# Performance work log

Measured on AMD Instinct MI355X. Metric: run time of the kernel, lower is better.

Reference implementation:

```python
import jax, jax.numpy as jnp
import numpy as np

HID, SD, EXP, DTR = 1024, 16, 2048, 64
B_, T_ = 4, 2048


def setup_inputs() -> dict:
    key = jax.random.key(0)
    ks = jax.random.split(key, 9)
    def rn(k, shape, s=0.02):
        return jax.random.normal(k, shape, jnp.float32) * s
    return {
        "x": jax.random.normal(ks[0], (B_, T_, HID), jnp.float32),
        "ln_g": jnp.ones((HID,), jnp.float32),
        "ln_b": jnp.zeros((HID,), jnp.float32),
        "W_in": rn(ks[1], (HID, 2 * EXP)),
        "b_in": jnp.zeros((2 * EXP,), jnp.float32),
        "W_del": rn(ks[2], (EXP, DTR)),
        "b_del": jnp.zeros((DTR,), jnp.float32),
        "W_dt": rn(ks[3], (DTR, EXP)),
        "b_dt": jnp.zeros((EXP,), jnp.float32),
        "W_B": rn(ks[4], (EXP, SD)),
        "b_B": jnp.zeros((SD,), jnp.float32),
        "W_C": rn(ks[5], (EXP, SD)),
        "b_C": jnp.zeros((SD,), jnp.float32),
        "A_log": -jnp.exp(0.1 * jax.random.normal(ks[6], (EXP, SD), jnp.float32)),
        "Dp": jnp.zeros((EXP,), jnp.float32),
        "W_out": rn(ks[7], (EXP, HID)),
        "b_out": jnp.zeros((HID,), jnp.float32),
    }


def _layernorm(x, g, b, eps=1e-5):
    m = jnp.mean(x, axis=-1, keepdims=True)
    v = jnp.var(x, axis=-1, keepdims=True)
    return (x - m) * jax.lax.rsqrt(v + eps) * g + b


def _selective_scan(u, delta, A, Bm, Cm):
    # u, delta: (B,T,E); Bm, Cm: (B,T,Sd); A: (E,Sd)
    def step(h, inp):
        u_t, d_t, B_t, C_t = inp  # (B,E),(B,E),(B,Sd),(B,Sd)
        A_disc = jnp.exp(d_t[..., None] * A[None])          # (B,E,Sd)
        h = A_disc * h + d_t[..., None] * B_t[:, None, :] * u_t[..., None]
        y_t = jnp.einsum("bs,bds->bd", C_t, h)
        return h, y_t
    h0 = jnp.zeros((u.shape[0], u.shape[2], A.shape[1]), u.dtype)
    xs = (u.transpose(1, 0, 2), delta.transpose(1, 0, 2),
          Bm.transpose(1, 0, 2), Cm.transpose(1, 0, 2))
    _, ys = jax.lax.scan(step, h0, xs)  # ys: (T,B,E)
    return ys.transpose(1, 0, 2)


def reference(x, ln_g, ln_b, W_in, b_in, W_del, b_del, W_dt, b_dt,
              W_B, b_B, W_C, b_C, A_log, Dp, W_out, b_out):
    res = x
    xn = _layernorm(x, ln_g, ln_b)
    xp = xn @ W_in + b_in                 # (B,T,2E)
    u, gate = jnp.split(xp, 2, axis=-1)   # each (B,T,E)
    u = jax.nn.silu(u)
    delta = jax.nn.softplus((u @ W_del + b_del) @ W_dt + b_dt)  # (B,T,E)
    Bm = u @ W_B + b_B                    # (B,T,Sd)
    Cm = u @ W_C + b_C                    # (B,T,Sd)
    A = -jnp.exp(A_log)                   # (E,Sd)
    y = _selective_scan(u, delta, A, Bm, Cm)
    y = y + u * Dp
    y = y * jax.nn.silu(gate)
    return y @ W_out + b_out + res
```

## Files before the change

kernel.cpp:

```cpp
#include <hip/hip_runtime.h>

#define HIDN 1024
#define EXPN 2048
#define SDIM 16
#define DTRN 64
#define BBN  4
#define TTN  2048
#define MMN  (BBN*TTN)
#define NCHUNK 32
#define CLEN (TTN/NCHUNK)
#define KSPL 8
#define KCH  (EXPN/KSPL)

typedef unsigned short u16;
typedef __bf16 bf16x8 __attribute__((ext_vector_type(8)));
typedef float f32x4 __attribute__((ext_vector_type(4)));

static __device__ __forceinline__ float b2f(u16 u) {
    union { unsigned int i; float f; } cv; cv.i = ((unsigned int)u) << 16; return cv.f;
}
static __device__ __forceinline__ u16 f2b(float f) {
    union { float f; unsigned int i; } cv; cv.f = f;
    unsigned int x = cv.i;
    return (u16)((x + 0x7fffu + ((x >> 16) & 1u)) >> 16);
}
static __device__ __forceinline__ float fexp2(float x) {
    return __builtin_amdgcn_exp2f(x);
}

static __device__ __forceinline__
void tr_tile(const float* __restrict__ W, u16* __restrict__ Wt,
             int K, int N, int bk, int bn, float (*t)[65]) {
    const int r0 = threadIdx.x >> 4, c0 = (threadIdx.x & 15) << 2;
    #pragma unroll
    for (int i = 0; i < 4; ++i) {
        float4 v = *(const float4*)(W + (size_t)(bk + r0 + i * 16) * N + bn + c0);
        t[r0 + i * 16][c0 + 0] = v.x; t[r0 + i * 16][c0 + 1] = v.y;
        t[r0 + i * 16][c0 + 2] = v.z; t[r0 + i * 16][c0 + 3] = v.w;
    }
    __syncthreads();
    #pragma unroll
    for (int i = 0; i < 4; ++i) {
        const int n = r0 + i * 16;
        ushort4 o;
        o.x = f2b(t[c0 + 0][n]); o.y = f2b(t[c0 + 1][n]);
        o.z = f2b(t[c0 + 2][n]); o.w = f2b(t[c0 + 3][n]);
        *(ushort4*)(Wt + (size_t)(bn + n) * K + bk + c0) = o;
    }
}

__global__ __launch_bounds__(256)
void k_prep(const float* __restrict__ W_in, const float* __restrict__ W_out,
            const float* __restrict__ W_dt, const float* __restrict__ W_del,
            const float* __restrict__ W_B, const float* __restrict__ W_C,
            const float* __restrict__ A_log,
            u16* __restrict__ Wt_in, u16* __restrict__ Wt_out,
            u16* __restrict__ Wdt_t, u16* __restrict__ Wcat,
            float* __restrict__ A2) {
    __shared__ float t[64][65];
    int blk = blockIdx.x;
    if (blk < 1024) {
        tr_tile(W_in, Wt_in, HIDN, 2 * EXPN, (blk >> 6) << 6, (blk & 63) << 6, t);
        return;
    }
    blk -= 1024;
    if (blk < 512) {
        tr_tile(W_out, Wt_out, EXPN, HIDN, (blk >> 4) << 6, (blk & 15) << 6, t);
        return;
    }
    blk -= 512;
    if (blk < 32) {
        tr_tile(W_dt, Wdt_t, DTRN, EXPN, 0, blk << 6, t);
        return;
    }
    blk -= 32;
    if (blk < 768) {
        const int i = blk * 256 + threadIdx.x;
        const int n = i >> 11, k = i & 2047;
        float v;
        if (n < 64)      v = W_del[(size_t)k * DTRN + n];
        else if (n < 80) v = W_B[(size_t)k * SDIM + (n - 64)];
        else             v = W_C[(size_t)k * SDIM + (n - 80)];
        Wcat[i] = f2b(v);
        return;
    }
    blk -= 768;
    {
        const int i = blk * 256 + threadIdx.x;
        A2[i] = -__expf(A_log[i]) * 1.44269504088896340736f;
    }
}

__global__ __launch_bounds__(256) void k_ln(const float* __restrict__ x,
                                            const float* __restrict__ g,
                                            const float* __restrict__ bta,
                                            u16* __restrict__ xn) {
    const int row = blockIdx.x, tid = threadIdx.x;
    const float4 xv = ((const float4*)(x + (size_t)row * HIDN))[tid];
    float s  = xv.x + xv.y + xv.z + xv.w;
    float ss = fmaf(xv.x, xv.x, fmaf(xv.y, xv.y, fmaf(xv.z, xv.z, xv.w * xv.w)));
    #pragma unroll
    for (int o = 32; o > 0; o >>= 1) { s += __shfl_down(s, o); ss += __shfl_down(ss, o); }
    __shared__ float as[4], bs[4];
    const int wid = tid >> 6, lane = tid & 63;
    if (lane == 0) { as[wid] = s; bs[wid] = ss; }
    __syncthreads();
    const float S  = as[0] + as[1] + as[2] + as[3];
    const float SS = bs[0] + bs[1] + bs[2] + bs[3];
    const float mean = S * (1.f / HIDN);
    const float var  = SS * (1.f / HIDN) - mean * mean;
    const float r = rsqrtf(var + 1e-5f);
    const float4 gv = ((const float4*)g)[tid];
    const float4 bv = ((const float4*)bta)[tid];
    ushort4 o;
    o.x = f2b((xv.x - mean) * r * gv.x + bv.x);
    o.y = f2b((xv.y - mean) * r * gv.y + bv.y);
    o.z = f2b((xv.z - mean) * r * gv.z + bv.z);
    o.w = f2b((xv.w - mean) * r * gv.w + bv.w);
    ((ushort4*)(xn + (size_t)row * HIDN))[tid] = o;
}

#define MEPI_SPLIT_SILU 0
#define MEPI_OUT        1
#define MEPI_SP         2

static __device__ __forceinline__
void stage256(const u16* __restrict__ A, const u16* __restrict__ Bt,
              u16 (*seg)[8192], int brow, int bcol, int K, int k0,
              const int* srow, const int* scol, int tid) {
    #pragma unroll
    for (int j = 0; j < 2; ++j) {
        #pragma unroll
        for (int h = 0; h < 2; ++h) {
            const u16* sa = A + (size_t)(brow + h * 128 + srow[j]) * K + k0 + scol[j];
            __builtin_amdgcn_global_load_lds(
                (const __attribute__((address_space(1))) void*)sa,
                (__attribute__((address_space(3))) void*)&seg[h][(j * 512 + tid) * 8], 16, 0, 0);
            const u16* sb = Bt + (size_t)(bcol + h * 128 + srow[j]) * K + k0 + scol[j];
            __builtin_amdgcn_global_load_lds(
                (const __attribute__((address_space(1))) void*)sb,
                (__attribute__((address_space(3))) void*)&seg[2 + h][(j * 512 + tid) * 8], 16, 0, 0);
        }
    }
}

template<int EPI>
__global__ __launch_bounds__(512, 2)
void mgemm256(const u16* __restrict__ A, const u16* __restrict__ Bt,
              const float* __restrict__ bias, void* __restrict__ O0,
              void* __restrict__ O1, const float* __restrict__ res,
              int N, int K) {
    __shared__ u16 lds[2][4][8192];
    const int tid  = threadIdx.x;
    const int lane = tid & 63, wid = tid >> 6;
    const int wm = wid >> 2, wn = wid & 3;
    const int r  = lane & 15, kh = lane >> 4;
    const int brow = blockIdx.y * 256, bcol = blockIdx.x * 256;

    int srow[2], scol[2];
    #pragma unroll
    for (int j = 0; j < 2; ++j) {
        const int q = j * 512 + tid;
        const int sub = q >> 6, qi = q & 63;
        const int qis = qi ^ (((qi >> 5) & 1) << 1);
        srow[j] = (sub >> 1) * 16 + (qi >> 2);
        scol[j] = ((sub & 1) << 5) + (qis & 3) * 8;
    }
    const int swz_kh = kh ^ (((r >> 3) & 1) << 1);
    const int rbase  = r * 32 + swz_kh * 8;
    const int bq     = wn & 1;

    f32x4 acc[8][4];
    #pragma unroll
    for (int i = 0; i < 8; ++i)
        #pragma unroll
        for (int n = 0; n < 4; ++n) acc[i][n] = (f32x4){0.f, 0.f, 0.f, 0.f};

    const int NT = K >> 6;
    stage256(A, Bt, lds[0], brow, bcol, K, 0, srow, scol, tid);
    stage256(A, Bt, lds[1], brow, bcol, K, 64, srow, scol, tid);
    asm volatile("s_waitcnt vmcnt(8)" ::: "memory");
    __builtin_amdgcn_s_barrier();
    asm volatile("" ::: "memory");

    bf16x8 a[4][2], b[2][2][2];
    for (int kt = 0; kt < NT; ++kt) {
        const u16* segA = lds[kt & 1][wm];
        const u16* segB = lds[kt & 1][2 + (wn >> 1)];
        #pragma unroll
        for (int mf = 0; mf < 4; ++mf)
            #pragma unroll
            for (int kk = 0; kk < 2; ++kk)
                a[mf][kk] = *(const bf16x8*)&segA[(mf * 2 + kk) * 512 + rbase];
        #pragma unroll
        for (int nf = 0; nf < 2; ++nf)
            #pragma unroll
            for (int kk = 0; kk < 2; ++kk)
                b[0][nf][kk] = *(const bf16x8*)&segB[((bq * 4 + nf) * 2 + kk) * 512 + rbase];
        __builtin_amdgcn_s_barrier(); asm volatile("" ::: "memory");
        __builtin_amdgcn_s_setprio(1);
        #pragma unroll
        for (int mf = 0; mf < 4; ++mf)
            #pragma unroll
            for (int nf = 0; nf < 2; ++nf)
                #pragma unroll
                for (int kk = 0; kk < 2; ++kk)
                    acc[mf][nf] = __builtin_amdgcn_mfma_f32_16x16x32_bf16(a[mf][kk], b[0][nf][kk], acc[mf][nf], 0, 0, 0);
        __builtin_amdgcn_s_setprio(0);
        __builtin_amdgcn_s_barrier(); asm volatile("" ::: "memory");
        #pragma unroll
        for (int nf = 0; nf < 2; ++nf)
            #pragma unroll
            for (int kk = 0; kk < 2; ++kk)
                b[1][nf][kk] = *(const bf16x8*)&segB[((bq * 4 + 2 + nf) * 2 + kk) * 512 + rbase];
        __builtin_amdgcn_s_barrier(); asm volatile("" ::: "memory");
        __builtin_amdgcn_s_setprio(1);
        #pragma unroll
        for (int mf = 0; mf < 4; ++mf)
            #pragma unroll
            for (int nf = 0; nf < 2; ++nf)
                #pragma unroll
                for (int kk = 0; kk < 2; ++kk)
                    acc[mf][2 + nf] = __builtin_amdgcn_mfma_f32_16x16x32_bf16(a[mf][kk], b[1][nf][kk], acc[mf][2 + nf], 0, 0, 0);
        __builtin_amdgcn_s_setprio(0);
        __builtin_amdgcn_s_barrier(); asm volatile("" ::: "memory");
        #pragma unroll
        for (int mf = 0; mf < 4; ++mf)
            #pragma unroll
            for (int kk = 0; kk < 2; ++kk)
                a[mf][kk] = *(const bf16x8*)&segA[((4 + mf) * 2 + kk) * 512 + rbase];
        __builtin_amdgcn_s_barrier(); asm volatile("" ::: "memory");
        __builtin_amdgcn_s_setprio(1);
        #pragma unroll
        for (int mf = 0; mf < 4; ++mf)
            #pragma unroll
            for (int nf = 0; nf < 2; ++nf)
                #pragma unroll
                for (int kk = 0; kk < 2; ++kk)
                    acc[4 + mf][nf] = __builtin_amdgcn_mfma_f32_16x16x32_bf16(a[mf][kk], b[0][nf][kk], acc[4 + mf][nf], 0, 0, 0);
        __builtin_amdgcn_s_setprio(0);
        __builtin_amdgcn_s_barrier(); asm volatile("" ::: "memory");
        if (kt + 2 < NT)
            stage256(A, Bt, lds[kt & 1], brow, bcol, K, (kt + 2) * 64, srow, scol, tid);
        __builtin_amdgcn_s_setprio(1);
        #pragma unroll
        for (int mf = 0; mf < 4; ++mf)
            #pragma unroll
            for (int nf = 0; nf < 2; ++nf)
                #pragma unroll
                for (int kk = 0; kk < 2; ++kk)
                    acc[4 + mf][2 + nf] = __builtin_amdgcn_mfma_f32_16x16x32_bf16(a[mf][kk], b[1][nf][kk], acc[4 + mf][2 + nf], 0, 0, 0);
        __builtin_amdgcn_s_setprio(0);
        if (kt + 2 < NT) { asm volatile("s_waitcnt vmcnt(8)" ::: "memory"); }
        else             { asm volatile("s_waitcnt vmcnt(0)" ::: "memory"); }
        __builtin_amdgcn_s_barrier(); asm volatile("" ::: "memory");
    }

    const int orow = brow + wm * 128 + kh * 4;
    const int ocol = bcol + wn * 64 + r;
    if constexpr (EPI == MEPI_SPLIT_SILU) {
        u16* dst; int cb;
        if (bcol < EXPN) { dst = (u16*)O0; cb = ocol; }
        else             { dst = (u16*)O1; cb = ocol - EXPN; }
        #pragma unroll
        for (int Mf = 0; Mf < 8; ++Mf)
            #pragma unroll
            for (int Nf = 0; Nf < 4; ++Nf)
                #pragma unroll
                for (int j = 0; j < 4; ++j) {
                    const int row = orow + Mf * 16 + j;
                    const int col = ocol + Nf * 16;
                    float v = acc[Mf][Nf][j] + bias[col];
                    float sv = v * (1.f / (1.f + __expf(-v)));
                    dst[(size_t)row * EXPN + cb + Nf * 16] = f2b(sv);
                }
    } else {
        float* o = (float*)O0;
        #pragma unroll
        for (int Mf = 0; Mf < 8; ++Mf)
            #pragma unroll
            for (int Nf = 0; Nf < 4; ++Nf)
                #pragma unroll
                for (int j = 0; j < 4; ++j) {
                    const int row = orow + Mf * 16 + j;
                    const int col = ocol + Nf * 16;
                    o[(size_t)row * N + col] = acc[Mf][Nf][j] + bias[col] + res[(size_t)row * N + col];
                }
    }
}

template<int EPI>
__global__ __launch_bounds__(256)
void mgemm(const u16* __restrict__ A, const u16* __restrict__ Bt,
           const float* __restrict__ bias, void* __restrict__ O0,
           void* __restrict__ O1, const float* __restrict__ res,
           int N, int K) {
    __shared__ u16 As[128 * 32];
    __shared__ u16 Bs[128 * 32];
    const int tid  = threadIdx.x;
    const int wave = tid >> 6, lane = tid & 63;
    const int brow = blockIdx.y * 128, bcol = blockIdx.x * 128;
    const int wm = wave >> 1, wn = wave & 1;
    const int r  = lane & 15, kh = lane >> 4;

    f32x4 acc[4][4];
    #pragma unroll
    for (int m = 0; m < 4; m++)
        #pragma unroll
        for (int n = 0; n < 4; n++) acc[m][n] = (f32x4){0.f, 0.f, 0.f, 0.f};

    const u16* ga0 = A  + (size_t)(brow +      (tid >> 2)) * K + (tid & 3) * 8;
    const u16* ga1 = A  + (size_t)(brow + 64 + (tid >> 2)) * K + (tid & 3) * 8;
    const u16* gb0 = Bt + (size_t)(bcol +      (tid >> 2)) * K + (tid & 3) * 8;
    const u16* gb1 = Bt + (size_t)(bcol + 64 + (tid >> 2)) * K + (tid & 3) * 8;
    u16* lA0 = As + (wave * 64) * 8;
    u16* lA1 = As + (256 + wave * 64) * 8;
    u16* lB0 = Bs + (wave * 64) * 8;
    u16* lB1 = Bs + (256 + wave * 64) * 8;

    for (int k0 = 0; k0 < K; k0 += 32) {
        __syncthreads();
        __builtin_amdgcn_global_load_lds((const __attribute__((address_space(1))) void*)(ga0 + k0),
                                         (__attribute__((address_space(3))) void*)lA0, 16, 0, 0);
        __builtin_amdgcn_global_load_lds((const __attribute__((address_space(1))) void*)(ga1 + k0),
                                         (__attribute__((address_space(3))) void*)lA1, 16, 0, 0);
        __builtin_amdgcn_global_load_lds((const __attribute__((address_space(1))) void*)(gb0 + k0),
                                         (__attribute__((address_space(3))) void*)lB0, 16, 0, 0);
        __builtin_amdgcn_global_load_lds((const __attribute__((address_space(1))) void*)(gb1 + k0),
                                         (__attribute__((address_space(3))) void*)lB1, 16, 0, 0);
        __syncthreads();
        bf16x8 af[4], bfr[4];
        #pragma unroll
        for (int mf = 0; mf < 4; ++mf)
            af[mf] = *(const bf16x8*)(As + ((wm * 64 + mf * 16 + r) * 32 + kh * 8));
        #pragma unroll
        for (int nf = 0; nf < 4; ++nf)
            bfr[nf] = *(const bf16x8*)(Bs + ((wn * 64 + nf * 16 + r) * 32 + kh * 8));
        #pragma unroll
        for (int mf = 0; mf < 4; ++mf)
            #pragma unroll
            for (int nf = 0; nf < 4; ++nf)
                acc[mf][nf] = __builtin_amdgcn_mfma_f32_16x16x32_bf16(af[mf], bfr[nf], acc[mf][nf], 0, 0, 0);
    }

    const int orow = brow + wm * 64 + kh * 4;
    const int ocol = bcol + wn * 64 + r;
    if constexpr (EPI == MEPI_SPLIT_SILU) {
        u16* dst; int cb;
        if (bcol < EXPN) { dst = (u16*)O0; cb = ocol; }
        else             { dst = (u16*)O1; cb = ocol - EXPN; }
        #pragma unroll
        for (int mf = 0; mf < 4; ++mf)
            #pragma unroll
            for (int nf = 0; nf < 4; ++nf)
                #pragma unroll
                for (int j = 0; j < 4; ++j) {
                    const int row = orow + mf * 16 + j;
                    const int col = ocol + nf * 16;
                    float v = acc[mf][nf][j] + bias[col];
                    float sv = v * (1.f / (1.f + __expf(-v)));
                    dst[(size_t)row * EXPN + cb + nf * 16] = f2b(sv);
                }
    } else if constexpr (EPI == MEPI_SP) {
        u16* o = (u16*)O0;
        #pragma unroll
        for (int mf = 0; mf < 4; ++mf)
            #pragma unroll
            for (int nf = 0; nf < 4; ++nf)
                #pragma unroll
                for (int j = 0; j < 4; ++j) {
                    const int row = orow + mf * 16 + j;
                    const int col = ocol + nf * 16;
                    float v = acc[mf][nf][j] + bias[col];
                    float sp = (v > 20.f) ? v
                             : 0.69314718056f * __builtin_amdgcn_logf(
                                   1.f + fexp2(1.44269504089f * v));
                    o[(size_t)row * N + col] = f2b(sp);
                }
    } else {
        float* o = (float*)O0;
        #pragma unroll
        for (int mf = 0; mf < 4; ++mf)
            #pragma unroll
            for (int nf = 0; nf < 4; ++nf)
                #pragma unroll
                for (int j = 0; j < 4; ++j) {
                    const int row = orow + mf * 16 + j;
                    const int col = ocol + nf * 16;
                    o[(size_t)row * N + col] = acc[mf][nf][j] + bias[col] + res[(size_t)row * N + col];
                }
    }
}

__global__ __launch_bounds__(256)
void k_proj(const u16* __restrict__ A, const u16* __restrict__ Wcat,
            float* __restrict__ Ppart) {
    __shared__ u16 As[128 * 32];
    __shared__ u16 Bs[96 * 32];
    const int tid  = threadIdx.x;
    const int wave = tid >> 6, lane = tid & 63;
    const int brow = blockIdx.y * 128;
    const int ks   = blockIdx.x;
    const int r = lane & 15, kh = lane >> 4;

    f32x4 acc[2][6];
    #pragma unroll
    for (int m = 0; m < 2; m++)
        #pragma unroll
        for (int n = 0; n < 6; n++) acc[m][n] = (f32x4){0.f, 0.f, 0.f, 0.f};

    const u16* ga0 = A + (size_t)(brow +      (tid >> 2)) * EXPN + ks * KCH + (tid & 3) * 8;
    const u16* ga1 = A + (size_t)(brow + 64 + (tid >> 2)) * EXPN + ks * KCH + (tid & 3) * 8;
    const u16* gb0 = Wcat + (size_t)(tid >> 2) * EXPN + ks * KCH + (tid & 3) * 8;
    const u16* gb1 = Wcat + (size_t)(64 + (tid >> 2)) * EXPN + ks * KCH + (tid & 3) * 8;
    u16* lA0 = As + (wave * 64) * 8;
    u16* lA1 = As + (256 + wave * 64) * 8;
    u16* lB0 = Bs + (wave * 64) * 8;
    u16* lB1 = Bs + (256 + wave * 64) * 8;

    for (int k0 = 0; k0 < KCH; k0 += 32) {
        __syncthreads();
        __builtin_amdgcn_global_load_lds((const __attribute__((address_space(1))) void*)(ga0 + k0),
                                         (__attribute__((address_space(3))) void*)lA0, 16, 0, 0);
        __builtin_amdgcn_global_load_lds((const __attribute__((address_space(1))) void*)(ga1 + k0),
                                         (__attribute__((address_space(3))) void*)lA1, 16, 0, 0);
        __builtin_amdgcn_global_load_lds((const __attribute__((address_space(1))) void*)(gb0 + k0),
                                         (__attribute__((address_space(3))) void*)lB0, 16, 0, 0);
        if (tid < 128)
            __builtin_amdgcn_global_load_lds((const __attribute__((address_space(1))) void*)(gb1 + k0),
                                             (__attribute__((address_space(3))) void*)lB1, 16, 0, 0);
        __syncthreads();
        bf16x8 af[2], bfr[6];
        #pragma unroll
        for (int mf = 0; mf < 2; ++mf)
            af[mf] = *(const bf16x8*)(As + ((wave * 32 + mf * 16 + r) * 32 + kh * 8));
        #pragma unroll
        for (int nf = 0; nf < 6; ++nf)
            bfr[nf] = *(const bf16x8*)(Bs + ((nf * 16 + r) * 32 + kh * 8));
        #pragma unroll
        for (int mf = 0; mf < 2; ++mf)
            #pragma unroll
            for (int nf = 0; nf < 6; ++nf)
                acc[mf][nf] = __builtin_amdgcn_mfma_f32_16x16x32_bf16(af[mf], bfr[nf], acc[mf][nf], 0, 0, 0);
    }
    const int orow = brow + wave * 32 + kh * 4;
    #pragma unroll
    for (int mf = 0; mf < 2; ++mf)
        #pragma unroll
        for (int nf = 0; nf < 6; ++nf)
            #pragma unroll
            for (int j = 0; j < 4; ++j)
                Ppart[((size_t)ks * MMN + orow + mf * 16 + j) * 96 + nf * 16 + r] = acc[mf][nf][j];
}

__global__ __launch_bounds__(192)
void k_red(const float* __restrict__ Ppart, const float* __restrict__ b_del,
           const float* __restrict__ b_B, const float* __restrict__ b_C,
           u16* __restrict__ t1b, float* __restrict__ Bm, float* __restrict__ Cm) {
    const int tid = threadIdx.x;
    const int ri  = tid / 96, col = tid - ri * 96;
    const int row = blockIdx.x * 2 + ri;
    float s = 0.f;
    #pragma unroll
    for (int ks = 0; ks < KSPL; ++ks)
        s += Ppart[((size_t)ks * MMN + row) * 96 + col];
    if (col < 64)      t1b[(size_t)row * DTRN + col] = f2b(s + b_del[col]);
    else if (col < 80) Bm[(size_t)row * SDIM + col - 64] = s + b_B[col - 64];
    else               Cm[(size_t)row * SDIM + col - 80] = s + b_C[col - 80];
}

__global__ __launch_bounds__(256)
void k_scan1(const u16* __restrict__ ub, const u16* __restrict__ db,
             const float* __restrict__ Bm, const float* __restrict__ A2,
             float* __restrict__ hend, float* __restrict__ Pp) {
    const int e = blockIdx.x * 256 + threadIdx.x;
    const int c = blockIdx.y, b = blockIdx.z;
    float a2[SDIM], h[SDIM];
    {
        const float4* ap = (const float4*)(A2 + (size_t)e * SDIM);
        float4 v0 = ap[0], v1 = ap[1], v2 = ap[2], v3 = ap[3];
        a2[0]=v0.x; a2[1]=v0.y; a2[2]=v0.z; a2[3]=v0.w;
        a2[4]=v1.x; a2[5]=v1.y; a2[6]=v1.z; a2[7]=v1.w;
        a2[8]=v2.x; a2[9]=v2.y; a2[10]=v2.z; a2[11]=v2.w;
        a2[12]=v3.x; a2[13]=v3.y; a2[14]=v3.z; a2[15]=v3.w;
    }
    #pragma unroll
    for (int s = 0; s < SDIM; s++) h[s] = 0.f;
    float sumd = 0.f;
    const int t0 = c * CLEN;
    size_t rb = ((size_t)b * TTN + t0) * EXPN + e;
    size_t bb_ = ((size_t)b * TTN + t0) * SDIM;
    for (int tt = 0; tt < CLEN; ++tt) {
        const float d  = b2f(db[rb]);
        const float uv = b2f(ub[rb]);
        const float4* bp = (const float4*)(Bm + bb_);
        float4 b0 = bp[0], b1 = bp[1], b2v = bp[2], b3 = bp[3];
        float bv[SDIM] = { b0.x,b0.y,b0.z,b0.w, b1.x,b1.y,b1.z,b1.w,
                           b2v.x,b2v.y,b2v.z,b2v.w, b3.x,b3.y,b3.z,b3.w };
        const float du = d * uv;
        sumd += d;
        #pragma unroll
        for (int s = 0; s < SDIM; ++s) {
            float ad = fexp2(d * a2[s]);
            h[s] = fmaf(ad, h[s], du * bv[s]);
        }
        rb += EXPN; bb_ += SDIM;
    }
    size_t ob = ((size_t)(b * NCHUNK + c) * SDIM) * EXPN + e;
    #pragma unroll
    for (int s = 0; s < SDIM; ++s) {
        hend[ob + (size_t)s * EXPN] = h[s];
        Pp  [ob + (size_t)s * EXPN] = fexp2(a2[s] * sumd);
    }
}

__global__ __launch_bounds__(256)
void k_fix(const float* __restrict__ hend, const float* __restrict__ Pp,
           float* __restrict__ hinit) {
    const int i = blockIdx.x * 256 + threadIdx.x;
    const int b = blockIdx.y;
    float hi = 0.f;
    size_t base = ((size_t)b * NCHUNK) * SDIM * EXPN + i;
    for (int cc = 0; cc < NCHUNK; ++cc) {
        size_t idx = base + (size_t)cc * SDIM * EXPN;
        hinit[idx] = hi;
        hi = fmaf(Pp[idx], hi, hend[idx]);
    }
}

__global__ __launch_bounds__(256)
void k_scan2(const u16* __restrict__ ub, const u16* __restrict__ db,
             const u16* __restrict__ sgb, const float* __restrict__ Bm,
             const float* __restrict__ Cm, const float* __restrict__ A2,
             const float* __restrict__ hinit, const float* __restrict__ Dp,
             u16* __restrict__ yb) {
    const int e = blockIdx.x * 256 + threadIdx.x;
    const int c = blockIdx.y, b = blockIdx.z;
    float a2[SDIM], h[SDIM];
    {
        const float4* ap = (const float4*)(A2 + (size_t)e * SDIM);
        float4 v0 = ap[0], v1 = ap[1], v2 = ap[2], v3 = ap[3];
        a2[0]=v0.x; a2[1]=v0.y; a2[2]=v0.z; a2[3]=v0.w;
        a2[4]=v1.x; a2[5]=v1.y; a2[6]=v1.z; a2[7]=v1.w;
        a2[8]=v2.x; a2[9]=v2.y; a2[10]=v2.z; a2[11]=v2.w;
        a2[12]=v3.x; a2[13]=v3.y; a2[14]=v3.z; a2[15]=v3.w;
    }
    {
        size_t hb = ((size_t)(b * NCHUNK + c) * SDIM) * EXPN + e;
        #pragma unroll
        for (int s = 0; s < SDIM; s++) h[s] = hinit[hb + (size_t)s * EXPN];
    }
    const float dpe = Dp[e];
    const int t0 = c * CLEN;
    size_t rb = ((size_t)b * TTN + t0) * EXPN + e;
    size_t bb_ = ((size_t)b * TTN + t0) * SDIM;
    for (int tt = 0; tt < CLEN; ++tt) {
        const float d   = b2f(db[rb]);
        const float uv  = b2f(ub[rb]);
        const float sgv = b2f(sgb[rb]);
        const float4* bp = (const float4*)(Bm + bb_);
        const float4* cp = (const float4*)(Cm + bb_);
        float4 b0 = bp[0], b1 = bp[1], b2v = bp[2], b3 = bp[3];
        float4 c0 = cp[0], c1 = cp[1], c2v = cp[2], c3 = cp[3];
        float bv[SDIM] = { b0.x,b0.y,b0.z,b0.w, b1.x,b1.y,b1.z,b1.w,
                           b2v.x,b2v.y,b2v.z,b2v.w, b3.x,b3.y,b3.z,b3.w };
        float cv[SDIM] = { c0.x,c0.y,c0.z,c0.w, c1.x,c1.y,c1.z,c1.w,
                           c2v.x,c2v.y,c2v.z,c2v.w, c3.x,c3.y,c3.z,c3.w };
        const float du = d * uv;
        float yt = 0.f;
        #pragma unroll
        for (int s = 0; s < SDIM; ++s) {
            float ad = fexp2(d * a2[s]);
            h[s] = fmaf(ad, h[s], du * bv[s]);
            yt = fmaf(cv[s], h[s], yt);
        }
        yb[rb] = f2b(fmaf(uv, dpe, yt) * sgv);
        rb += EXPN; bb_ += SDIM;
    }
}

extern "C" void kernel_launch(void* const* d_in, const int* in_sizes, int n_in,
                              void* d_out, int out_size, void* d_ws, size_t ws_size,
                              hipStream_t stream) {
    const float* x     = (const float*)d_in[0];
    const float* ln_g  = (const float*)d_in[1];
    const float* ln_b  = (const float*)d_in[2];
    const float* W_in  = (const float*)d_in[3];
    const float* b_in  = (const float*)d_in[4];
    const float* W_del = (const float*)d_in[5];
    const float* b_del = (const float*)d_in[6];
    const float* W_dt  = (const float*)d_in[7];
    const float* b_dt  = (const float*)d_in[8];
    const float* W_B   = (const float*)d_in[9];
    const float* b_B   = (const float*)d_in[10];
    const float* W_C   = (const float*)d_in[11];
    const float* b_C   = (const float*)d_in[12];
    const float* A_log = (const float*)d_in[13];
    const float* Dp    = (const float*)d_in[14];
    const float* W_out = (const float*)d_in[15];
    const float* b_out = (const float*)d_in[16];
    float* out = (float*)d_out;

    char* p = (char*)d_ws;
    auto alloc = [&](size_t bytes) {
        char* r = p; p += (bytes + 255) & ~(size_t)255; return (void*)r;
    };
    u16* xn   = (u16*)alloc((size_t)MMN * HIDN * 2);
    u16* u    = (u16*)alloc((size_t)MMN * EXPN * 2);
    u16* sg   = (u16*)alloc((size_t)MMN * EXPN * 2);
    u16* dl   = (u16*)alloc((size_t)MMN * EXPN * 2);
    u16* y    = (u16*)alloc((size_t)MMN * EXPN * 2);
    u16* t1b  = (u16*)alloc((size_t)MMN * DTRN * 2);
    float* Bm = (float*)alloc((size_t)MMN * SDIM * 4);
    float* Cm = (float*)alloc((size_t)MMN * SDIM * 4);
    float* A2 = (float*)alloc((size_t)EXPN * SDIM * 4);
    u16* Wt_in  = (u16*)alloc((size_t)(2 * EXPN) * HIDN * 2);
    u16* Wt_out = (u16*)alloc((size_t)HIDN * EXPN * 2);
    u16* Wcat   = (u16*)alloc((size_t)96 * EXPN * 2);
    u16* Wdt_t  = (u16*)alloc((size_t)EXPN * DTRN * 2);
    const size_t hsz = (size_t)BBN * NCHUNK * EXPN * SDIM * 4;
    float* hend  = (float*)alloc(hsz);
    float* Pp    = (float*)alloc(hsz);
    float* hinit = (float*)alloc(hsz);
    float* Ppart = hend;

    k_prep<<<dim3(1024 + 512 + 32 + 768 + 128), 256, 0, stream>>>(
        W_in, W_out, W_dt, W_del, W_B, W_C, A_log, Wt_in, Wt_out, Wdt_t, Wcat, A2);
    k_ln<<<dim3(MMN), 256, 0, stream>>>(x, ln_g, ln_b, xn);

    mgemm256<MEPI_SPLIT_SILU><<<dim3(2 * EXPN / 256, MMN / 256), 512, 0, stream>>>(
        xn, Wt_in, b_in, u, sg, nullptr, 2 * EXPN, HIDN);
    k_proj<<<dim3(KSPL, MMN / 128), 256, 0, stream>>>(u, Wcat, Ppart);
    k_red<<<dim3(MMN / 2), 192, 0, stream>>>(Ppart, b_del, b_B, b_C, t1b, Bm, Cm);
    mgemm<MEPI_SP><<<dim3(EXPN / 128, MMN / 128), 256, 0, stream>>>(
        t1b, Wdt_t, b_dt, dl, nullptr, nullptr, EXPN, DTRN);
    k_scan1<<<dim3(EXPN / 256, NCHUNK, BBN), 256, 0, stream>>>(u, dl, Bm, A2, hend, Pp);
    k_fix<<<dim3(SDIM * EXPN / 256, BBN), 256, 0, stream>>>(hend, Pp, hinit);
    k_scan2<<<dim3(EXPN / 256, NCHUNK, BBN), 256, 0, stream>>>(u, dl, sg, Bm, Cm, A2, hinit, Dp, y);
    mgemm<MEPI_OUT><<<dim3(HIDN / 128, MMN / 128), 256, 0, stream>>>(
        y, Wt_out, b_out, out, nullptr, x, HIDN, EXPN);
}
```

Before: 307.1 us.

## Simplify 256-tile GEMM inner loop and make scan threads handle two channels

The big in-projection GEMM drops the four-phase barrier-separated schedule. It now loads all B fragments and half of A, issues 32 MFMAs, loads the other half of A and issues 32 more, with one barrier before staging the next tile. Both scan kernels now give each thread two adjacent channels, using paired bf16 and float2 loads and stores and halving the grid. This amortises the per-timestep B/C loads across two channels and adds ILP, but it raises register pressure and halves the number of scan blocks, and the GEMM loses its fine-grained overlap of LDS reads with MFMAs.

```diff
diff --git a/kernel.cpp b/kernel.cpp
--- a/kernel.cpp
+++ b/kernel.cpp
@@ -183,76 +183,50 @@
     __builtin_amdgcn_s_barrier();
     asm volatile("" ::: "memory");
 
-    bf16x8 a[4][2], b[2][2][2];
     for (int kt = 0; kt < NT; ++kt) {
         const u16* segA = lds[kt & 1][wm];
         const u16* segB = lds[kt & 1][2 + (wn >> 1)];
-        #pragma unroll
-        for (int mf = 0; mf < 4; ++mf)
+        bf16x8 b[4][2], a0[4][2], a1[4][2];
+        #pragma unroll
+        for (int nf = 0; nf < 4; ++nf)
             #pragma unroll
             for (int kk = 0; kk < 2; ++kk)
-                a[mf][kk] = *(const bf16x8*)&segA[(mf * 2 + kk) * 512 + rbase];
-        #pragma unroll
-        for (int nf = 0; nf < 2; ++nf)
+                b[nf][kk] = *(const bf16x8*)&segB[((bq * 4 + nf) * 2 + kk) * 512 + rbase];
+        #pragma unroll
+        for (int mf = 0; mf < 4; ++mf)
             #pragma unroll
             for (int kk = 0; kk < 2; ++kk)
-                b[0][nf][kk] = *(const bf16x8*)&segB[((bq * 4 + nf) * 2 + kk) * 512 + rbase];
-        __builtin_amdgcn_s_barrier(); asm volatile("" ::: "memory");
+                a0[mf][kk] = *(const bf16x8*)&segA[(mf * 2 + kk) * 512 + rbase];
         __builtin_amdgcn_s_setprio(1);
         #pragma unroll
         for (int mf = 0; mf < 4; ++mf)
             #pragma unroll
-            for (int nf = 0; nf < 2; ++nf)
+            for (int nf = 0; nf < 4; ++nf)
                 #pragma unroll
                 for (int kk = 0; kk < 2; ++kk)
-                    acc[mf][nf] = __builtin_amdgcn_mfma_f32_16x16x32_bf16(a[mf][kk], b[0][nf][kk], acc[mf][nf], 0, 0, 0);
+                    acc[mf][nf] = __builtin_amdgcn_mfma_f32_16x16x32_bf16(a0[mf][kk], b[nf][kk], acc[mf][nf], 0, 0, 0);
+        __builtin_amdgcn_s_setprio(0);
+        #pragma unroll
+        for (int mf = 0; mf < 4; ++mf)
+            #pragma unroll
+            for (int kk = 0; kk < 2; ++kk)
+                a1[mf][kk] = *(const bf16x8*)&segA[((4 + mf) * 2 + kk) * 512 + rbase];
+        __builtin_amdgcn_s_setprio(1);
+        #pragma unroll
+        for (int mf = 0; mf < 4; ++mf)
+            #pragma unroll
+            for (int nf = 0; nf < 4; ++nf)
+                #pragma unroll
+                for (int kk = 0; kk < 2; ++kk)
+                    acc[4 + mf][nf] = __builtin_amdgcn_mfma_f32_16x16x32_bf16(a1[mf][kk], b[nf][kk], acc[4 + mf][nf], 0, 0, 0);
         __builtin_amdgcn_s_setprio(0);
         __builtin_amdgcn_s_barrier(); asm volatile("" ::: "memory");
-        #pragma unroll
-        for (int nf = 0; nf < 2; ++nf)
-            #pragma unroll
-            for (int kk = 0; kk < 2; ++kk)
-                b[1][nf][kk] = *(const bf16x8*)&segB[((bq * 4 + 2 + nf) * 2 + kk) * 512 + rbase];
-        __builtin_amdgcn_s_barrier(); asm volatile("" ::: "memory");
-        __builtin_amdgcn_s_setprio(1);
-        #pragma unroll
-        for (int mf = 0; mf < 4; ++mf)
-            #pragma unroll
-            for (int nf = 0; nf < 2; ++nf)
-                #pragma unroll
-                for (int kk = 0; kk < 2; ++kk)
-                    acc[mf][2 + nf] = __builtin_amdgcn_mfma_f32_16x16x32_bf16(a[mf][kk], b[1][nf][kk], acc[mf][2 + nf], 0, 0, 0);
-        __builtin_amdgcn_s_setprio(0);
-        __builtin_amdgcn_s_barrier(); asm volatile("" ::: "memory");
-        #pragma unroll
-        for (int mf = 0; mf < 4; ++mf)
-            #pragma unroll
-            for (int kk = 0; kk < 2; ++kk)
-                a[mf][kk] = *(const bf16x8*)&segA[((4 + mf) * 2 + kk) * 512 + rbase];
-        __builtin_amdgcn_s_barrier(); asm volatile("" ::: "memory");
-        __builtin_amdgcn_s_setprio(1);
-        #pragma unroll
-        for (int mf = 0; mf < 4; ++mf)
-            #pragma unroll
-            for (int nf = 0; nf < 2; ++nf)
-                #pragma unroll
-                for (int kk = 0; kk < 2; ++kk)
-                    acc[4 + mf][nf] = __builtin_amdgcn_mfma_f32_16x16x32_bf16(a[mf][kk], b[0][nf][kk], acc[4 + mf][nf], 0, 0, 0);
-        __builtin_amdgcn_s_setprio(0);
-        __builtin_amdgcn_s_barrier(); asm volatile("" ::: "memory");
-        if (kt + 2 < NT)
+        if (kt + 2 < NT) {
             stage256(A, Bt, lds[kt & 1], brow, bcol, K, (kt + 2) * 64, srow, scol, tid);
-        __builtin_amdgcn_s_setprio(1);
-        #pragma unroll
-        for (int mf = 0; mf < 4; ++mf)
-            #pragma unroll
-            for (int nf = 0; nf < 2; ++nf)
-                #pragma unroll
-                for (int kk = 0; kk < 2; ++kk)
-                    acc[4 + mf][2 + nf] = __builtin_amdgcn_mfma_f32_16x16x32_bf16(a[mf][kk], b[1][nf][kk], acc[4 + mf][2 + nf], 0, 0, 0);
-        __builtin_amdgcn_s_setprio(0);
-        if (kt + 2 < NT) { asm volatile("s_waitcnt vmcnt(8)" ::: "memory"); }
-        else             { asm volatile("s_waitcnt vmcnt(0)" ::: "memory"); }
+            asm volatile("s_waitcnt vmcnt(8)" ::: "memory");
+        } else {
+            asm volatile("s_waitcnt vmcnt(0)" ::: "memory");
+        }
         __builtin_amdgcn_s_barrier(); asm volatile("" ::: "memory");
     }
 
@@ -473,44 +447,53 @@
 void k_scan1(const u16* __restrict__ ub, const u16* __restrict__ db,
              const float* __restrict__ Bm, const float* __restrict__ A2,
              float* __restrict__ hend, float* __restrict__ Pp) {
-    const int e = blockIdx.x * 256 + threadIdx.x;
+    const int e = (blockIdx.x * 256 + threadIdx.x) * 2;
     const int c = blockIdx.y, b = blockIdx.z;
-    float a2[SDIM], h[SDIM];
-    {
-        const float4* ap = (const float4*)(A2 + (size_t)e * SDIM);
-        float4 v0 = ap[0], v1 = ap[1], v2 = ap[2], v3 = ap[3];
-        a2[0]=v0.x; a2[1]=v0.y; a2[2]=v0.z; a2[3]=v0.w;
-        a2[4]=v1.x; a2[5]=v1.y; a2[6]=v1.z; a2[7]=v1.w;
-        a2[8]=v2.x; a2[9]=v2.y; a2[10]=v2.z; a2[11]=v2.w;
-        a2[12]=v3.x; a2[13]=v3.y; a2[14]=v3.z; a2[15]=v3.w;
-    }
-    #pragma unroll
-    for (int s = 0; s < SDIM; s++) h[s] = 0.f;
-    float sumd = 0.f;
+    float a2[2][SDIM], h[2][SDIM];
+    #pragma unroll
+    for (int p = 0; p < 2; ++p) {
+        const float4* ap = (const float4*)(A2 + (size_t)(e + p) * SDIM);
+        #pragma unroll
+        for (int q = 0; q < 4; ++q) {
+            float4 v = ap[q];
+            a2[p][q*4+0] = v.x; a2[p][q*4+1] = v.y;
+            a2[p][q*4+2] = v.z; a2[p][q*4+3] = v.w;
+        }
+    }
+    #pragma unroll
+    for (int p = 0; p < 2; ++p)
+        #pragma unroll
+        for (int s = 0; s < SDIM; ++s) h[p][s] = 0.f;
+    float sumd0 = 0.f, sumd1 = 0.f;
     const int t0 = c * CLEN;
     size_t rb = ((size_t)b * TTN + t0) * EXPN + e;
     size_t bb_ = ((size_t)b * TTN + t0) * SDIM;
     for (int tt = 0; tt < CLEN; ++tt) {
-        const float d  = b2f(db[rb]);
-        const float uv = b2f(ub[rb]);
+        const ushort2 dv = *(const ushort2*)(db + rb);
+        const ushort2 uv = *(const ushort2*)(ub + rb);
         const float4* bp = (const float4*)(Bm + bb_);
-        float4 b0 = bp[0], b1 = bp[1], b2v = bp[2], b3 = bp[3];
-        float bv[SDIM] = { b0.x,b0.y,b0.z,b0.w, b1.x,b1.y,b1.z,b1.w,
-                           b2v.x,b2v.y,b2v.z,b2v.w, b3.x,b3.y,b3.z,b3.w };
-        const float du = d * uv;
-        sumd += d;
+        float bv[SDIM];
+        #pragma unroll
+        for (int q = 0; q < 4; ++q) {
+            float4 v = bp[q];
+            bv[q*4+0]=v.x; bv[q*4+1]=v.y; bv[q*4+2]=v.z; bv[q*4+3]=v.w;
+        }
+        const float d0 = b2f(dv.x), d1 = b2f(dv.y);
+        const float du0 = d0 * b2f(uv.x), du1 = d1 * b2f(uv.y);
+        sumd0 += d0; sumd1 += d1;
         #pragma unroll
         for (int s = 0; s < SDIM; ++s) {
-            float ad = fexp2(d * a2[s]);
-            h[s] = fmaf(ad, h[s], du * bv[s]);
+            h[0][s] = fmaf(fexp2(d0 * a2[0][s]), h[0][s], du0 * bv[s]);
+            h[1][s] = fmaf(fexp2(d1 * a2[1][s]), h[1][s], du1 * bv[s]);
         }
         rb += EXPN; bb_ += SDIM;
     }
     size_t ob = ((size_t)(b * NCHUNK + c) * SDIM) * EXPN + e;
     #pragma unroll
     for (int s = 0; s < SDIM; ++s) {
-        hend[ob + (size_t)s * EXPN] = h[s];
-        Pp  [ob + (size_t)s * EXPN] = fexp2(a2[s] * sumd);
+        *(float2*)(hend + ob + (size_t)s * EXPN) = make_float2(h[0][s], h[1][s]);
+        *(float2*)(Pp   + ob + (size_t)s * EXPN) =
+            make_float2(fexp2(a2[0][s] * sumd0), fexp2(a2[1][s] * sumd1));
     }
 }
 
@@ -534,47 +517,60 @@
              const float* __restrict__ Cm, const float* __restrict__ A2,
              const float* __restrict__ hinit, const float* __restrict__ Dp,
              u16* __restrict__ yb) {
-    const int e = blockIdx.x * 256 + threadIdx.x;
+    const int e = (blockIdx.x * 256 + threadIdx.x) * 2;
     const int c = blockIdx.y, b = blockIdx.z;
-    float a2[SDIM], h[SDIM];
-    {
-        const float4* ap = (const float4*)(A2 + (size_t)e * SDIM);
-        float4 v0 = ap[0], v1 = ap[1], v2 = ap[2], v3 = ap[3];
-        a2[0]=v0.x; a2[1]=v0.y; a2[2]=v0.z; a2[3]=v0.w;
-        a2[4]=v1.x; a2[5]=v1.y; a2[6]=v1.z; a2[7]=v1.w;
-        a2[8]=v2.x; a2[9]=v2.y; a2[10]=v2.z; a2[11]=v2.w;
-        a2[12]=v3.x; a2[13]=v3.y; a2[14]=v3.z; a2[15]=v3.w;
+    float a2[2][SDIM], h[2][SDIM];
+    #pragma unroll
+    for (int p = 0; p < 2; ++p) {
+        const float4* ap = (const float4*)(A2 + (size_t)(e + p) * SDIM);
+        #pragma unroll
+        for (int q = 0; q < 4; ++q) {
+            float4 v = ap[q];
+            a2[p][q*4+0] = v.x; a2[p][q*4+1] = v.y;
+            a2[p][q*4+2] = v.z; a2[p][q*4+3] = v.w;
+        }
     }
     {
         size_t hb = ((size_t)(b * NCHUNK + c) * SDIM) * EXPN + e;
         #pragma unroll
-        for (int s = 0; s < SDIM; s++) h[s] = hinit[hb + (size_t)s * EXPN];
-    }
-    const float dpe = Dp[e];
+        for (int s = 0; s < SDIM; ++s) {
+            float2 hv = *(const float2*)(hinit + hb + (size_t)s * EXPN);
+            h[0][s] = hv.x; h[1][s] = hv.y;
+        }
+    }
+    const float dpe0 = Dp[e], dpe1 = Dp[e + 1];
     const int t0 = c * CLEN;
     size_t rb = ((size_t)b * TTN + t0) * EXPN + e;
     size_t bb_ = ((size_t)b * TTN + t0) * SDIM;
     for (int tt = 0; tt < CLEN; ++tt) {
-        const float d   = b2f(db[rb]);
-        const float uv  = b2f(ub[rb]);
-        const float sgv = b2f(sgb[rb]);
+        const ushort2 dv  = *(const ushort2*)(db + rb);
+        const ushort2 uv  = *(const ushort2*)(ub + rb);
+        const ushort2 sgv = *(const ushort2*)(sgb + rb);
         const float4* bp = (const float4*)(Bm + bb_);
         const float4* cp = (const float4*)(Cm + bb_);
-        float4 b0 = bp[0], b1 = bp[1], b2v = bp[2], b3 = bp[3];
-        float4 c0 = cp[0], c1 = cp[1], c2v = cp[2], c3 = cp[3];
-        float bv[SDIM] = { b0.x,b0.y,b0.z,b0.w, b1.x,b1.y,b1.z,b1.w,
-                           b2v.x,b2v.y,b2v.z,b2v.w, b3.x,b3.y,b3.z,b3.w };
-        float cv[SDIM] = { c0.x,c0.y,c0.z,c0.w, c1.x,c1.y,c1.z,c1.w,
-                           c2v.x,c2v.y,c2v.z,c2v.w, c3.x,c3.y,c3.z,c3.w };
-        const float du = d * uv;
-        float yt = 0.f;
+        float bv[SDIM], cv[SDIM];
+        #pragma unroll
+        for (int q = 0; q < 4; ++q) {
+            float4 v = bp[q];
+            bv[q*4+0]=v.x; bv[q*4+1]=v.y; bv[q*4+2]=v.z; bv[q*4+3]=v.w;
+            float4 w = cp[q];
+            cv[q*4+0]=w.x; cv[q*4+1]=w.y; cv[q*4+2]=w.z; cv[q*4+3]=w.w;
+        }
+        const float d0 = b2f(dv.x), d1 = b2f(dv.y);
+        const float u0 = b2f(uv.x), u1 = b2f(uv.y);
+        const float du0 = d0 * u0, du1 = d1 * u1;
+        float yt0 = 0.f, yt1 = 0.f;
         #pragma unroll
         for (int s = 0; s < SDIM; ++s) {
-            float ad = fexp2(d * a2[s]);
-            h[s] = fmaf(ad, h[s], du * bv[s]);
-            yt = fmaf(cv[s], h[s], yt);
-        }
-        yb[rb] = f2b(fmaf(uv, dpe, yt) * sgv);
+            h[0][s] = fmaf(fexp2(d0 * a2[0][s]), h[0][s], du0 * bv[s]);
+            yt0 = fmaf(cv[s], h[0][s], yt0);
+            h[1][s] = fmaf(fexp2(d1 * a2[1][s]), h[1][s], du1 * bv[s]);
+            yt1 = fmaf(cv[s], h[1][s], yt1);
+        }
+        ushort2 o;
+        o.x = f2b(fmaf(u0, dpe0, yt0) * b2f(sgv.x));
+        o.y = f2b(fmaf(u1, dpe1, yt1) * b2f(sgv.y));
+        *(ushort2*)(yb + rb) = o;
         rb += EXPN; bb_ += SDIM;
     }
 }
@@ -634,9 +630,9 @@
     k_red<<<dim3(MMN / 2), 192, 0, stream>>>(Ppart, b_del, b_B, b_C, t1b, Bm, Cm);
     mgemm<MEPI_SP><<<dim3(EXPN / 128, MMN / 128), 256, 0, stream>>>(
         t1b, Wdt_t, b_dt, dl, nullptr, nullptr, EXPN, DTRN);
-    k_scan1<<<dim3(EXPN / 256, NCHUNK, BBN), 256, 0, stream>>>(u, dl, Bm, A2, hend, Pp);
+    k_scan1<<<dim3(EXPN / 512, NCHUNK, BBN), 256, 0, stream>>>(u, dl, Bm, A2, hend, Pp);
     k_fix<<<dim3(SDIM * EXPN / 256, BBN), 256, 0, stream>>>(hend, Pp, hinit);
-    k_scan2<<<dim3(EXPN / 256, NCHUNK, BBN), 256, 0, stream>>>(u, dl, sg, Bm, Cm, A2, hinit, Dp, y);
+    k_scan2<<<dim3(EXPN / 512, NCHUNK, BBN), 256, 0, stream>>>(u, dl, sg, Bm, Cm, A2, hinit, Dp, y);
     mgemm<MEPI_OUT><<<dim3(HIDN / 128, MMN / 128), 256, 0, stream>>>(
         y, Wt_out, b_out, out, nullptr, x, HIDN, EXPN);
 }
```

After: 319.6 us. 1.04x slower.
